# Kernel tuning notes

Hardware: AMD Instinct MI355X
Metric: run time of the kernel (lower is better)

The kernel has to match this reference:

```python
import jax, jax.numpy as jnp
import numpy as np

B, N, K, S_IN, S_OUT, C, FD = 32, 325, 20, 12, 12, 10, 64
ALPHA = 0.5  # LeakyReLU negative slope

def leaky(x):
    return jnp.where(x >= 0, x, ALPHA * x)

def setup_inputs() -> dict:
    key = jax.random.key(0)
    ks = jax.random.split(key, 9)
    s = 0.2
    return {
        "fushed_features": jax.random.normal(ks[0], (B, N, FD), jnp.float32),
        "input_data": jax.random.normal(ks[1], (B, N, S_IN), jnp.float32),
        "w_W": jax.random.normal(ks[2], (S_IN, S_OUT), jnp.float32) * s,
        "w_b": jax.random.normal(ks[3], (S_OUT,), jnp.float32) * s,
        "a1_W": jax.random.normal(ks[4], (2 * S_OUT, 4 * S_OUT), jnp.float32) * s,
        "a1_b": jax.random.normal(ks[5], (4 * S_OUT,), jnp.float32) * s,
        "a2_W": jax.random.normal(ks[6], (4 * S_OUT, C), jnp.float32) * s,
        "a2_b": jax.random.normal(ks[7], (C,), jnp.float32) * s,
        "adj_mx_topk_index": jax.random.randint(ks[8], (B, N, K), 0, N),
    }

def reference(fushed_features, input_data, w_W, w_b, a1_W, a1_b, a2_W, a2_b, adj_mx_topk_index):
    # w_net: Linear + LeakyReLU -> wh [B,N,S_OUT]
    wh = leaky(input_data @ w_W + w_b)
    # a_net on cat([wh_i, wh_j]): split first linear to avoid materializing [B,N,N,2*S_OUT]
    hx = wh @ a1_W[:S_OUT]   # contribution of wh_x (row node i)
    hy = wh @ a1_W[S_OUT:]   # contribution of wh_y (col node j)
    hidden = leaky(hx[:, :, None, :] + hy[:, None, :, :] + a1_b)   # [B,N,N,4*S_OUT]
    attention = leaky(hidden @ a2_W + a2_b)                        # [B,N,N,C]
    idx = adj_mx_topk_index                                        # [B,N,K]
    # gather top-k neighbors along dim 2
    idx_c = jnp.broadcast_to(idx[..., None], idx.shape + (attention.shape[-1],))
    attention_mask = jnp.take_along_axis(attention, idx_c, axis=2)  # [B,N,K,C]
    attention_mask = jax.nn.softmax(attention_mask, axis=-1)
    # gather neighbor features: wh_expand_top_k[b,i,k] = wh[b, idx[b,i,k]]
    wh_topk = wh[jnp.arange(wh.shape[0])[:, None, None], idx]       # [B,N,K,S_OUT]
    # output = attention_mask^T @ wh_topk
    output_data = jnp.einsum('bnkc,bnks->bncs', attention_mask, wh_topk)
    # clustering loss on detached neighbor features (cosine similarity)
    wt = jax.lax.stop_gradient(wh_topk)
    wtn = wt / (jnp.linalg.norm(wt, axis=-1, keepdims=True) + 1e-8)
    dist_mat = jnp.einsum('bnks,bnls->bnkl', wtn, wtn)              # [B,N,K,K]
    same = (dist_mat >= 0.5).astype(dist_mat.dtype)
    diff = 1.0 - same
    prob = jnp.einsum('bnkc,bnlc->bnkl', attention_mask, attention_mask)
    prob = jnp.clip(prob, 1e-4, 1.0 - 1e-4)
    logp = jnp.log(prob)
    cl = -(same * logp - diff * logp)
    cluster_loss = (cl.sum((-1, -2)) - jnp.trace(cl, axis1=-2, axis2=-1)).mean()
    return output_data, cluster_loss, dist_mat.mean(), wh.mean()
```

## Files before the change

kernel.cpp:

```cpp
#include <hip/hip_runtime.h>
#include <math.h>

#define Bdim 32
#define Ndim 325
#define Kdim 20
#define Sdim 12
#define Cdim 10
#define Hdim 48
#define NB   (Bdim*Ndim)
#define OUT_SCALARS (NB*Cdim*Sdim)
#define Tpairs (Kdim*(Kdim-1)/2)
#define BN_BLOCKS (NB/4)

#define O_WH  0
#define O_HX  (O_WH + NB*Sdim)
#define O_HY  (O_HX + NB*Hdim)
#define O_PCL (O_HY + NB*Hdim)
#define O_PDS (O_PCL + BN_BLOCKS)
#define O_PWH (O_PDS + BN_BLOCKS)
#define O_ATT (O_PWH + NB)
#define WS_BASE_FLOATS (O_ATT + NB*Kdim*12)

__device__ __forceinline__ float leaky(float x) { return x >= 0.f ? x : 0.5f * x; }

__global__ __launch_bounds__(256)
void node_kernel(const float* __restrict__ x,
                 const float* __restrict__ wW, const float* __restrict__ wb,
                 const float* __restrict__ A1, const float* __restrict__ b1,
                 float* __restrict__ ws)
{
    __shared__ float s_wh[4][Sdim];
    const int slot = threadIdx.x >> 6, lane = threadIdx.x & 63;
    const int node = blockIdx.x * 4 + slot;
    const float* xr = x + (size_t)node * Sdim;

    float v = 0.f;
    if (lane < Sdim) {
        float acc = wb[lane];
        #pragma unroll
        for (int i = 0; i < Sdim; i++) acc += xr[i] * wW[i * Sdim + lane];
        v = leaky(acc);
        s_wh[slot][lane] = v;
        ws[O_WH + (size_t)node * Sdim + lane] = v;
    }
    __syncthreads();

    #pragma unroll
    for (int rep = 0; rep < 2; rep++) {
        const int e = lane + rep * 64;
        if (e < 2 * Hdim) {
            const int which = e / Hdim, d = e - which * Hdim;
            float acc = which ? 0.f : b1[d];
            #pragma unroll
            for (int s = 0; s < Sdim; s++)
                acc += s_wh[slot][s] * A1[(which * Sdim + s) * Hdim + d];
            ws[(which ? O_HY : O_HX) + (size_t)node * Hdim + d] = acc;
        }
    }

    #pragma unroll
    for (int off = 32; off > 0; off >>= 1) v += __shfl_down(v, off);
    if (lane == 0) ws[O_PWH + node] = v;
}

__global__ __launch_bounds__(256)
void att_kernel(const int* __restrict__ topk,
                const float* __restrict__ A2, const float* __restrict__ b2,
                float* __restrict__ ws)
{
    const int gid = blockIdx.x * 256 + threadIdx.x;
    if (gid >= NB * Kdim) return;
    const int bn = gid / Kdim;
    const int b  = bn / Ndim;
    const int j  = topk[gid];

    const float4* hx4 = (const float4*)(ws + O_HX + (size_t)bn * Hdim);
    const float4* hy4 = (const float4*)(ws + O_HY + ((size_t)b * Ndim + j) * Hdim);

    float acc[Cdim];
    #pragma unroll
    for (int c = 0; c < Cdim; c++) acc[c] = b2[c];
    #pragma unroll
    for (int q = 0; q < 12; q++) {
        const float4 xv = hx4[q], yv = hy4[q];
        const float hh[4] = { leaky(xv.x + yv.x), leaky(xv.y + yv.y),
                              leaky(xv.z + yv.z), leaky(xv.w + yv.w) };
        #pragma unroll
        for (int i = 0; i < 4; i++) {
            #pragma unroll
            for (int c = 0; c < Cdim; c++)
                acc[c] += hh[i] * A2[(q * 4 + i) * Cdim + c];
        }
    }
    float m = -1e30f;
    #pragma unroll
    for (int c = 0; c < Cdim; c++) { acc[c] = leaky(acc[c]); m = fmaxf(m, acc[c]); }
    float sum = 0.f;
    #pragma unroll
    for (int c = 0; c < Cdim; c++) { acc[c] = __expf(acc[c] - m); sum += acc[c]; }
    const float inv = 1.f / sum;

    float* ar = ws + O_ATT + (size_t)gid * 12;
    *(float4*)(ar + 0) = make_float4(acc[0]*inv, acc[1]*inv, acc[2]*inv, acc[3]*inv);
    *(float4*)(ar + 4) = make_float4(acc[4]*inv, acc[5]*inv, acc[6]*inv, acc[7]*inv);
    *(float4*)(ar + 8) = make_float4(acc[8]*inv, acc[9]*inv, 0.f, 0.f);
}

__global__ __launch_bounds__(256)
void bn_kernel(const int* __restrict__ topk,
               float* __restrict__ ws, float* __restrict__ out)
{
    __shared__ float s_whj [4][Kdim][12];
    __shared__ float s_am  [4][Kdim][12];
    __shared__ float s_invn[4][Kdim];
    __shared__ int   s_idx [4][Kdim];
    __shared__ float s_red[2][4];

    const int tid = threadIdx.x;
    const int slot = tid >> 6, t = tid & 63;
    const int bn = blockIdx.x * 4 + slot, b = bn / Ndim;

    if (t < Kdim) s_idx[slot][t] = topk[(size_t)bn * Kdim + t];
    __syncthreads();

    if (t < 60) {
        const int k = t / 3, q = t - k * 3;
        const float4 v = *(const float4*)(ws + O_WH + ((size_t)b * Ndim + s_idx[slot][k]) * Sdim + q * 4);
        *(float4*)&s_whj[slot][k][q * 4] = v;
        const float4 a = *(const float4*)(ws + O_ATT + (size_t)bn * (Kdim * 12) + t * 4);
        *(float4*)&s_am[slot][k][q * 4] = a;
    }
    __syncthreads();

    float cl = 0.f, ds = 0.f;

    if (t < Kdim) {
        const float4 w0 = *(const float4*)&s_whj[slot][t][0];
        const float4 w1 = *(const float4*)&s_whj[slot][t][4];
        const float4 w2 = *(const float4*)&s_whj[slot][t][8];
        const float nn = w0.x*w0.x + w0.y*w0.y + w0.z*w0.z + w0.w*w0.w
                       + w1.x*w1.x + w1.y*w1.y + w1.z*w1.z + w1.w*w1.w
                       + w2.x*w2.x + w2.y*w2.y + w2.z*w2.z + w2.w*w2.w;
        const float invn = 1.f / (sqrtf(nn) + 1e-8f);
        s_invn[slot][t] = invn;
        ds += nn * invn * invn;
    } else if (t < Kdim + 30) {
        const int e = t - Kdim, c = e / 3, sq = e - c * 3;
        float4 o = make_float4(0.f, 0.f, 0.f, 0.f);
        #pragma unroll
        for (int k = 0; k < Kdim; k++) {
            const float a = s_am[slot][k][c];
            const float4 w = *(const float4*)&s_whj[slot][k][sq * 4];
            o.x += a * w.x; o.y += a * w.y; o.z += a * w.z; o.w += a * w.w;
        }
        *(float4*)(out + (size_t)bn * (Cdim * Sdim) + c * Sdim + sq * 4) = o;
    }
    __syncthreads();

    #pragma unroll
    for (int it = 0; it < 3; it++) {
        const int e = t + it * 64;
        if (e < Tpairs) {
            const int r = Tpairs - 1 - e;
            const int m = (int)((sqrtf((float)(8 * r + 1)) - 1.f) * 0.5f + 1e-4f);
            const int k = Kdim - 2 - m;
            const int l = Kdim - 1 - (r - (m * (m + 1)) / 2);

            const float4 a0 = *(const float4*)&s_whj[slot][k][0];
            const float4 a1 = *(const float4*)&s_whj[slot][k][4];
            const float4 a2 = *(const float4*)&s_whj[slot][k][8];
            const float4 c0 = *(const float4*)&s_whj[slot][l][0];
            const float4 c1 = *(const float4*)&s_whj[slot][l][4];
            const float4 c2 = *(const float4*)&s_whj[slot][l][8];
            const float draw = a0.x*c0.x + a0.y*c0.y + a0.z*c0.z + a0.w*c0.w
                             + a1.x*c1.x + a1.y*c1.y + a1.z*c1.z + a1.w*c1.w
                             + a2.x*c2.x + a2.y*c2.y + a2.z*c2.z + a2.w*c2.w;
            const float d = draw * s_invn[slot][k] * s_invn[slot][l];

            const float4 p0 = *(const float4*)&s_am[slot][k][0];
            const float4 p1 = *(const float4*)&s_am[slot][k][4];
            const float4 p2 = *(const float4*)&s_am[slot][k][8];
            const float4 q0 = *(const float4*)&s_am[slot][l][0];
            const float4 q1 = *(const float4*)&s_am[slot][l][4];
            const float4 q2 = *(const float4*)&s_am[slot][l][8];
            float p = p0.x*q0.x + p0.y*q0.y + p0.z*q0.z + p0.w*q0.w
                    + p1.x*q1.x + p1.y*q1.y + p1.z*q1.z + p1.w*q1.w
                    + p2.x*q2.x + p2.y*q2.y + p2.z*q2.z + p2.w*q2.w;

            p = fminf(fmaxf(p, 1e-4f), 1.f - 1e-4f);
            const float lp = __logf(p);
            ds += 2.f * d;
            cl += 2.f * ((d >= 0.5f) ? -lp : lp);
        }
    }

    #pragma unroll
    for (int off = 32; off > 0; off >>= 1) {
        cl += __shfl_down(cl, off);
        ds += __shfl_down(ds, off);
    }
    if (t == 0) { s_red[0][slot] = cl; s_red[1][slot] = ds; }
    __syncthreads();
    if (tid == 0) {
        ws[O_PCL + blockIdx.x] = s_red[0][0] + s_red[0][1] + s_red[0][2] + s_red[0][3];
        ws[O_PDS + blockIdx.x] = s_red[1][0] + s_red[1][1] + s_red[1][2] + s_red[1][3];
    }
}

__global__ __launch_bounds__(1024)
void finalize(const float* __restrict__ ws, float* __restrict__ out)
{
    const int t = threadIdx.x;
    float cl = 0.f, ds = 0.f, wm = 0.f;
    for (int i = t; i < BN_BLOCKS; i += 1024) {
        cl += ws[O_PCL + i]; ds += ws[O_PDS + i];
    }
    for (int i = t; i < NB; i += 1024) wm += ws[O_PWH + i];
    #pragma unroll
    for (int off = 32; off > 0; off >>= 1) {
        cl += __shfl_down(cl, off);
        ds += __shfl_down(ds, off);
        wm += __shfl_down(wm, off);
    }
    __shared__ float r[3][16];
    const int w = t >> 6, lane = t & 63;
    if (lane == 0) { r[0][w] = cl; r[1][w] = ds; r[2][w] = wm; }
    __syncthreads();
    if (t == 0) {
        float c = 0.f, d = 0.f, m = 0.f;
        #pragma unroll
        for (int i = 0; i < 16; i++) { c += r[0][i]; d += r[1][i]; m += r[2][i]; }
        out[OUT_SCALARS + 0] = c * (1.f / (float)NB);
        out[OUT_SCALARS + 1] = d * (1.f / ((float)NB * Kdim * Kdim));
        out[OUT_SCALARS + 2] = m * (1.f / ((float)NB * Sdim));
    }
}

__global__ void zero_scalars(float* out) {
    const int t = threadIdx.x;
    if (t < 3) out[OUT_SCALARS + t] = 0.f;
}

__global__ __launch_bounds__(64)
void fused_kernel(const float* __restrict__ input_data,
                  const float* __restrict__ w_W,  const float* __restrict__ w_b,
                  const float* __restrict__ a1_W, const float* __restrict__ a1_b,
                  const float* __restrict__ a2_W, const float* __restrict__ a2_b,
                  const int*   __restrict__ topk,
                  float* __restrict__ out)
{
    __shared__ float s_wW[Sdim * Sdim];
    __shared__ float s_wb[Sdim];
    __shared__ float s_A1[2 * Sdim * Hdim];
    __shared__ float s_b1[Hdim];
    __shared__ float s_A2f[Hdim * Cdim];
    __shared__ float s_b2f[Cdim];
    __shared__ float s_whs[Sdim];
    __shared__ float s_hx[Hdim];
    __shared__ float s_whj[Kdim][Sdim + 1];
    __shared__ float s_hid[Kdim][Hdim + 1];
    __shared__ float s_am [Kdim][Cdim + 1];
    __shared__ float s_wtn[Kdim][Sdim + 1];
    __shared__ int   s_idx[Kdim];

    const int t = threadIdx.x, bn = blockIdx.x, b = bn / Ndim;

    for (int i = t; i < Sdim * Sdim; i += 64)      s_wW[i] = w_W[i];
    if (t < Sdim)                                  s_wb[t] = w_b[t];
    for (int i = t; i < 2 * Sdim * Hdim; i += 64)  s_A1[i] = a1_W[i];
    if (t < Hdim)                                  s_b1[t] = a1_b[t];
    for (int i = t; i < Hdim * Cdim; i += 64)      s_A2f[i] = a2_W[i];
    if (t < Cdim)                                  s_b2f[t] = a2_b[t];
    if (t < Kdim)                                  s_idx[t] = topk[(size_t)bn * Kdim + t];
    __syncthreads();

    const float* xs = input_data + (size_t)bn * Sdim;
    if (t < Sdim) {
        float acc = s_wb[t];
        #pragma unroll
        for (int i = 0; i < Sdim; i++) acc += xs[i] * s_wW[i * Sdim + t];
        s_whs[t] = leaky(acc);
    }
    __syncthreads();

    if (t < Hdim) {
        float acc = 0.f;
        #pragma unroll
        for (int s = 0; s < Sdim; s++) acc += s_whs[s] * s_A1[s * Hdim + t];
        s_hx[t] = acc;
    }
    for (int e = t; e < Kdim * Sdim; e += 64) {
        const int k = e / Sdim, ss = e - k * Sdim;
        const float* xj = input_data + ((size_t)b * Ndim + s_idx[k]) * Sdim;
        float acc = s_wb[ss];
        #pragma unroll
        for (int i = 0; i < Sdim; i++) acc += xj[i] * s_wW[i * Sdim + ss];
        s_whj[k][ss] = leaky(acc);
    }
    __syncthreads();

    for (int e = t; e < Kdim * Hdim; e += 64) {
        const int k = e / Hdim, d = e - k * Hdim;
        float acc = s_hx[d] + s_b1[d];
        #pragma unroll
        for (int s = 0; s < Sdim; s++) acc += s_whj[k][s] * s_A1[(Sdim + s) * Hdim + d];
        s_hid[k][d] = leaky(acc);
    }
    __syncthreads();

    for (int e = t; e < Kdim * Cdim; e += 64) {
        const int k = e / Cdim, c = e - k * Cdim;
        float acc = s_b2f[c];
        #pragma unroll
        for (int d = 0; d < Hdim; d++) acc += s_hid[k][d] * s_A2f[d * Cdim + c];
        s_am[k][c] = leaky(acc);
    }
    __syncthreads();

    if (t < Kdim) {
        float m = -1e30f;
        #pragma unroll
        for (int c = 0; c < Cdim; c++) m = fmaxf(m, s_am[t][c]);
        float ex[Cdim]; float sum = 0.f;
        #pragma unroll
        for (int c = 0; c < Cdim; c++) { ex[c] = expf(s_am[t][c] - m); sum += ex[c]; }
        const float inv = 1.f / sum;
        #pragma unroll
        for (int c = 0; c < Cdim; c++) s_am[t][c] = ex[c] * inv;
        float nn = 0.f;
        #pragma unroll
        for (int s = 0; s < Sdim; s++) nn += s_whj[t][s] * s_whj[t][s];
        const float invn = 1.f / (sqrtf(nn) + 1e-8f);
        #pragma unroll
        for (int s = 0; s < Sdim; s++) s_wtn[t][s] = s_whj[t][s] * invn;
    }
    __syncthreads();

    float* op = out + (size_t)bn * (Cdim * Sdim);
    for (int e = t; e < Cdim * Sdim; e += 64) {
        const int c = e / Sdim, ss = e - c * Sdim;
        float acc = 0.f;
        #pragma unroll
        for (int k = 0; k < Kdim; k++) acc += s_am[k][c] * s_whj[k][ss];
        op[e] = acc;
    }

    float cl = 0.f, ds = 0.f;
    for (int e = t; e < Kdim * Kdim; e += 64) {
        const int k = e / Kdim, l = e - k * Kdim;
        float d = 0.f;
        #pragma unroll
        for (int s = 0; s < Sdim; s++) d += s_wtn[k][s] * s_wtn[l][s];
        ds += d;
        if (k != l) {
            float p = 0.f;
            #pragma unroll
            for (int c = 0; c < Cdim; c++) p += s_am[k][c] * s_am[l][c];
            p = fminf(fmaxf(p, 1e-4f), 1.f - 1e-4f);
            const float lp = logf(p);
            cl += (d >= 0.5f) ? -lp : lp;
        }
    }
    float whl = (t < Sdim) ? s_whs[t] : 0.f;
    #pragma unroll
    for (int off = 32; off > 0; off >>= 1) {
        cl  += __shfl_down(cl,  off);
        ds  += __shfl_down(ds,  off);
        whl += __shfl_down(whl, off);
    }
    if (t == 0) {
        atomicAdd(&out[OUT_SCALARS + 0], cl  * (1.f / (float)NB));
        atomicAdd(&out[OUT_SCALARS + 1], ds  * (1.f / ((float)NB * Kdim * Kdim)));
        atomicAdd(&out[OUT_SCALARS + 2], whl * (1.f / ((float)NB * Sdim)));
    }
}

extern "C" void kernel_launch(void* const* d_in, const int* in_sizes, int n_in,
                              void* d_out, int out_size, void* d_ws, size_t ws_size,
                              hipStream_t stream) {
    (void)in_sizes; (void)n_in; (void)out_size;
    const float* input_data = (const float*)d_in[1];
    const float* w_W  = (const float*)d_in[2];
    const float* w_b  = (const float*)d_in[3];
    const float* a1_W = (const float*)d_in[4];
    const float* a1_b = (const float*)d_in[5];
    const float* a2_W = (const float*)d_in[6];
    const float* a2_b = (const float*)d_in[7];
    const int*   topk = (const int*)d_in[8];
    float* out = (float*)d_out;
    float* ws  = (float*)d_ws;

    if (ws_size >= (size_t)WS_BASE_FLOATS * sizeof(float)) {
        hipLaunchKernelGGL(node_kernel, dim3(NB / 4), dim3(256), 0, stream,
                           input_data, w_W, w_b, a1_W, a1_b, ws);
        hipLaunchKernelGGL(att_kernel, dim3((NB * Kdim + 255) / 256), dim3(256), 0, stream,
                           topk, a2_W, a2_b, ws);
        hipLaunchKernelGGL(bn_kernel, dim3(BN_BLOCKS), dim3(256), 0, stream,
                           topk, ws, out);
        hipLaunchKernelGGL(finalize, dim3(1), dim3(1024), 0, stream, ws, out);
    } else {
        hipLaunchKernelGGL(zero_scalars, dim3(1), dim3(64), 0, stream, out);
        hipLaunchKernelGGL(fused_kernel, dim3(NB), dim3(64), 0, stream,
                           input_data, w_W, w_b, a1_W, a1_b, a2_W, a2_b, topk, out);
    }
}
```

Measured before the change: 110.8 us.

## Process 40 nodes per node_kernel block and use wave barriers in bn_kernel

node_kernel now handles 40 nodes per 256-thread block instead of 4 nodes with mostly idle lanes. Every thread now does useful work for the wh and hx/hy projections, and the wh-sum partials are reduced per block, so finalize reads 260 partials instead of 10400. In bn_kernel, the block-wide __syncthreads are replaced by wave barriers, since each 64-lane slot only touches its own shared-memory region. The aim is to cut idle lanes, launch and block overhead, and barrier stalls. It relies on each slot being exactly one wavefront for correctness.

```diff
diff --git a/kernel.cpp b/kernel.cpp
--- a/kernel.cpp
+++ b/kernel.cpp
@@ -11,6 +11,8 @@
 #define OUT_SCALARS (NB*Cdim*Sdim)
 #define Tpairs (Kdim*(Kdim-1)/2)
 #define BN_BLOCKS (NB/4)
+#define NODE_BLOCKS 260
+#define NPB 40
 
 #define O_WH  0
 #define O_HX  (O_WH + NB*Sdim)
@@ -18,7 +20,7 @@
 #define O_PCL (O_HY + NB*Hdim)
 #define O_PDS (O_PCL + BN_BLOCKS)
 #define O_PWH (O_PDS + BN_BLOCKS)
-#define O_ATT (O_PWH + NB)
+#define O_ATT (O_PWH + NODE_BLOCKS)
 #define WS_BASE_FLOATS (O_ATT + NB*Kdim*12)
 
 __device__ __forceinline__ float leaky(float x) { return x >= 0.f ? x : 0.5f * x; }
@@ -29,38 +31,50 @@
                  const float* __restrict__ A1, const float* __restrict__ b1,
                  float* __restrict__ ws)
 {
-    __shared__ float s_wh[4][Sdim];
-    const int slot = threadIdx.x >> 6, lane = threadIdx.x & 63;
-    const int node = blockIdx.x * 4 + slot;
-    const float* xr = x + (size_t)node * Sdim;
+    __shared__ float s_wh[NPB][Sdim];
+    __shared__ float s_r[4];
+    const int tid = threadIdx.x;
+    const int base = blockIdx.x * NPB;
 
     float v = 0.f;
-    if (lane < Sdim) {
-        float acc = wb[lane];
-        #pragma unroll
-        for (int i = 0; i < Sdim; i++) acc += xr[i] * wW[i * Sdim + lane];
-        v = leaky(acc);
-        s_wh[slot][lane] = v;
-        ws[O_WH + (size_t)node * Sdim + lane] = v;
-    }
-    __syncthreads();
-
     #pragma unroll
     for (int rep = 0; rep < 2; rep++) {
-        const int e = lane + rep * 64;
-        if (e < 2 * Hdim) {
-            const int which = e / Hdim, d = e - which * Hdim;
-            float acc = which ? 0.f : b1[d];
+        const int e = tid + rep * 256;
+        if (e < NPB * Sdim) {
+            const int n = e / Sdim, s = e - n * Sdim;
+            const float* xr = x + (size_t)(base + n) * Sdim;
+            float acc = wb[s];
             #pragma unroll
-            for (int s = 0; s < Sdim; s++)
-                acc += s_wh[slot][s] * A1[(which * Sdim + s) * Hdim + d];
-            ws[(which ? O_HY : O_HX) + (size_t)node * Hdim + d] = acc;
+            for (int i = 0; i < Sdim; i++) acc += xr[i] * wW[i * Sdim + s];
+            acc = leaky(acc);
+            s_wh[n][s] = acc;
+            ws[O_WH + (size_t)(base + n) * Sdim + s] = acc;
+            v += acc;
         }
     }
+    __syncthreads();
+
+    #pragma unroll
+    for (int rep = 0; rep < 15; rep++) {
+        const int e = tid + rep * 256;
+        const int n = e / 96, r = e - n * 96;
+        const int which = r / Hdim, d = r - which * Hdim;
+        const float4 w0 = *(const float4*)&s_wh[n][0];
+        const float4 w1 = *(const float4*)&s_wh[n][4];
+        const float4 w2 = *(const float4*)&s_wh[n][8];
+        const float* Ac = A1 + (which * Sdim) * Hdim + d;
+        float acc = which ? 0.f : b1[d];
+        acc += w0.x*Ac[0*Hdim] + w0.y*Ac[1*Hdim] + w0.z*Ac[2*Hdim] + w0.w*Ac[3*Hdim]
+             + w1.x*Ac[4*Hdim] + w1.y*Ac[5*Hdim] + w1.z*Ac[6*Hdim] + w1.w*Ac[7*Hdim]
+             + w2.x*Ac[8*Hdim] + w2.y*Ac[9*Hdim] + w2.z*Ac[10*Hdim] + w2.w*Ac[11*Hdim];
+        ws[(which ? O_HY : O_HX) + (size_t)(base + n) * Hdim + d] = acc;
+    }
 
     #pragma unroll
     for (int off = 32; off > 0; off >>= 1) v += __shfl_down(v, off);
-    if (lane == 0) ws[O_PWH + node] = v;
+    if ((tid & 63) == 0) s_r[tid >> 6] = v;
+    __syncthreads();
+    if (tid == 0) ws[O_PWH + blockIdx.x] = s_r[0] + s_r[1] + s_r[2] + s_r[3];
 }
 
 __global__ __launch_bounds__(256)
@@ -121,7 +135,7 @@
     const int bn = blockIdx.x * 4 + slot, b = bn / Ndim;
 
     if (t < Kdim) s_idx[slot][t] = topk[(size_t)bn * Kdim + t];
-    __syncthreads();
+    __builtin_amdgcn_wave_barrier();
 
     if (t < 60) {
         const int k = t / 3, q = t - k * 3;
@@ -130,7 +144,7 @@
         const float4 a = *(const float4*)(ws + O_ATT + (size_t)bn * (Kdim * 12) + t * 4);
         *(float4*)&s_am[slot][k][q * 4] = a;
     }
-    __syncthreads();
+    __builtin_amdgcn_wave_barrier();
 
     float cl = 0.f, ds = 0.f;
 
@@ -155,7 +169,7 @@
         }
         *(float4*)(out + (size_t)bn * (Cdim * Sdim) + c * Sdim + sq * 4) = o;
     }
-    __syncthreads();
+    __builtin_amdgcn_wave_barrier();
 
     #pragma unroll
     for (int it = 0; it < 3; it++) {
@@ -215,7 +229,7 @@
     for (int i = t; i < BN_BLOCKS; i += 1024) {
         cl += ws[O_PCL + i]; ds += ws[O_PDS + i];
     }
-    for (int i = t; i < NB; i += 1024) wm += ws[O_PWH + i];
+    if (t < NODE_BLOCKS) wm = ws[O_PWH + t];
     #pragma unroll
     for (int off = 32; off > 0; off >>= 1) {
         cl += __shfl_down(cl, off);
@@ -391,7 +405,7 @@
     float* ws  = (float*)d_ws;
 
     if (ws_size >= (size_t)WS_BASE_FLOATS * sizeof(float)) {
-        hipLaunchKernelGGL(node_kernel, dim3(NB / 4), dim3(256), 0, stream,
+        hipLaunchKernelGGL(node_kernel, dim3(NODE_BLOCKS), dim3(256), 0, stream,
                            input_data, w_W, w_b, a1_W, a1_b, ws);
         hipLaunchKernelGGL(att_kernel, dim3((NB * Kdim + 255) / 256), dim3(256), 0, stream,
                            topk, a2_W, a2_b, ws);
```

Measured after the change: 109.8 us. No clear change (-0.9%).
